# Kernel tuning notes

Hardware: AMD Instinct MI355X
Metric: run time of the kernel (lower is better)

Reference implementation:

```python
import jax, jax.numpy as jnp
import numpy as np
import math

DIM = 128
K = 64
OUT = 256
N, H, W = 32, 64, 64
EPS = 1e-12  # F.normalize clamp


def _l2norm(v, axis):
    n = jnp.sqrt(jnp.sum(v * v, axis=axis, keepdims=True))
    return v / jnp.maximum(n, EPS)


def setup_inputs() -> dict:
    key = jax.random.key(0)
    ks = jax.random.split(key, 6)
    s = 1.0 / math.sqrt(DIM)
    x = jax.random.normal(ks[0], (N, DIM, H, W), dtype=jnp.float32)
    cluster_centers = jax.random.uniform(ks[1], (K, DIM), dtype=jnp.float32) * s
    conv_w = jax.random.normal(ks[2], (K, DIM), dtype=jnp.float32) * s  # 1x1 conv kernel squeezed
    conv_b = jax.random.normal(ks[3], (K,), dtype=jnp.float32) * s
    mlp_w = jax.random.normal(ks[4], (OUT, K * DIM), dtype=jnp.float32) * s / math.sqrt(K * DIM)
    mlp_b = jax.random.normal(ks[5], (OUT,), dtype=jnp.float32) * s
    return {"x": x, "cluster_centers": cluster_centers, "conv_w": conv_w,
            "conv_b": conv_b, "mlp_w": mlp_w, "mlp_b": mlp_b}


def reference(x, cluster_centers, conv_w, conv_b, mlp_w, mlp_b):
    n, c, h, w = x.shape
    xf = x.reshape(n, c, h * w)                                   # [N,C,P]
    # 1x1 conv == per-pixel matmul
    logits = jnp.einsum('kc,ncp->nkp', conv_w, xf) + conv_b[None, :, None]
    a = jax.nn.softmax(logits, axis=1)                            # softmax over clusters, [N,K,P]
    # VLAD via algebraic identity (same math as broadcast-subtract-sum):
    # sum_p a[n,k,p]*(x[n,c,p] - centers[k,c])
    vlad = jnp.einsum('nkp,ncp->nkc', a, xf) \
           - a.sum(axis=-1)[..., None] * cluster_centers[None]    # [N,K,C]
    vlad = _l2norm(vlad, axis=2)            # intra-normalization over C
    vlad = vlad.reshape(n, -1)              # [N, K*C]
    vlad = _l2norm(vlad, axis=1)
    vlad = vlad @ mlp_w.T + mlp_b           # [N, OUT]
    vlad = _l2norm(vlad, axis=1)
    return vlad
```

## Files before the change

### kernel.cpp

```cpp
#include <hip/hip_runtime.h>
#include <math.h>


#define N_IMG 32
#define C_DIM 128
#define P_PIX 4096
#define K_CL  64
#define OUT_D 256

#define CHUNKS 8
#define NSUB 4
#define PART_ROW 132
#define PART_BLK (K_CL * PART_ROW)

typedef __attribute__((ext_vector_type(8))) short bf16x8;
typedef __attribute__((ext_vector_type(4))) short bf16x4;
typedef __attribute__((ext_vector_type(4))) float f32x4;
typedef __attribute__((ext_vector_type(2))) unsigned u32x2;
typedef __attribute__((ext_vector_type(4))) unsigned u32x4;

__device__ __forceinline__ unsigned cvtpk(float a, float b) {
    unsigned r;
    asm("v_cvt_pk_bf16_f32 %0, %1, %2" : "=v"(r) : "v"(a), "v"(b));
    return r;
}
__device__ __forceinline__ unsigned short bf1(float a) {
    union { float f; unsigned u; } x; x.f = a;
    return (unsigned short)((x.u + 0x7FFFu + ((x.u >> 16) & 1u)) >> 16);
}

__device__ __forceinline__ f32x4 mfma16(bf16x8 a, bf16x8 b, f32x4 c) {
    return __builtin_amdgcn_mfma_f32_16x16x32_bf16(a, b, c, 0, 0, 0);
}

__device__ __forceinline__ u32x2 tr16(unsigned addr) {
    u32x2 d;
    asm volatile("ds_read_b64_tr_b16 %0, %1" : "=v"(d) : "v"(addr));
    return d;
}
__device__ __forceinline__ u32x2 tr16_o1024(unsigned addr) {
    u32x2 d;
    asm volatile("ds_read_b64_tr_b16 %0, %1 offset:1024" : "=v"(d) : "v"(addr));
    return d;
}

__device__ __forceinline__ void bar_lgkm() {
    __builtin_amdgcn_sched_barrier(0);
    asm volatile("s_waitcnt lgkmcnt(0)" ::: "memory");
    __builtin_amdgcn_s_barrier();
    __builtin_amdgcn_sched_barrier(0);
}

template<int CTRL>
__device__ __forceinline__ float dppmv(float v) {
    union { float f; int i; } u; u.f = v;
    u.i = __builtin_amdgcn_update_dpp(u.i, u.i, CTRL, 0xF, 0xF, false);
    return u.f;
}
__device__ __forceinline__ float rowmax16(float v) {
    v = fmaxf(v, dppmv<0xB1>(v));
    v = fmaxf(v, dppmv<0x4E>(v));
    v = fmaxf(v, dppmv<0x141>(v));
    v = fmaxf(v, dppmv<0x140>(v));
    return v;
}
__device__ __forceinline__ float rowsum16(float v) {
    v += dppmv<0xB1>(v);
    v += dppmv<0x4E>(v);
    v += dppmv<0x141>(v);
    v += dppmv<0x140>(v);
    return v;
}

__global__ __launch_bounds__(512, 2)
void k_vlad_mfma(const float* __restrict__ x, const float* __restrict__ conv_w,
                 const float* __restrict__ conv_b, float* __restrict__ part)
{
    __shared__ short xc_s[16384];
    __shared__ short a_s[8192];
    __shared__ short w_s[8192];
    __shared__ float asred[512];

    const int t   = threadIdx.x;
    const int w   = t >> 6;
    const int l   = t & 63;
    const int l15 = l & 15;
    const int lg  = l >> 4;
    const int n   = blockIdx.x >> 3;
    const int ch  = blockIdx.x & 7;
    const int pb0 = ch * 512;

    const unsigned xc_base = (unsigned)(unsigned long long)(void*)xc_s;
    const float LOG2E = 1.44269504f;

    const float* xr0 = x + ((long)n * C_DIM + 16 * w + l15) * P_PIX;
    float4 raw[8];
#pragma unroll
    for (int ks = 0; ks < 4; ++ks) {
        const float* p = xr0 + pb0 + ks * 32 + lg * 8;
        raw[ks * 2 + 0] = *(const float4*)(p);
        raw[ks * 2 + 1] = *(const float4*)(p + 4);
    }

    {
        const int k = t >> 3, sub = t & 7;
        const float* wr = conv_w + k * C_DIM + sub * 16;
#pragma unroll
        for (int j = 0; j < 2; ++j) {
            float4 a = *(const float4*)(wr + j * 8);
            float4 b = *(const float4*)(wr + j * 8 + 4);
            union { u32x4 u; bf16x8 v; } cv;
            cv.u.x = cvtpk(a.x * LOG2E, a.y * LOG2E);
            cv.u.y = cvtpk(a.z * LOG2E, a.w * LOG2E);
            cv.u.z = cvtpk(b.x * LOG2E, b.y * LOG2E);
            cv.u.w = cvtpk(b.z * LOG2E, b.w * LOG2E);
            const int g = sub * 2 + j;
            const unsigned off = (unsigned)(k * 256 + ((g * 16) ^ ((k & 7) << 4)));
            *(bf16x8*)((char*)w_s + off) = cv.v;
        }
    }
    float bias[4];
#pragma unroll
    for (int nt = 0; nt < 4; ++nt) bias[nt] = conv_b[nt * 16 + l15] * LOG2E;

    bar_lgkm();

    bf16x8 wf[4][4];
#pragma unroll
    for (int nt = 0; nt < 4; ++nt)
#pragma unroll
        for (int ks = 0; ks < 4; ++ks) {
            const unsigned wb = (unsigned)((nt * 16 + l15) * 256
                + ((ks * 64 + lg * 16) ^ ((l15 & 7) << 4)));
            wf[nt][ks] = *(const bf16x8*)((char*)w_s + wb);
        }

    f32x4 acc2[4];
#pragma unroll
    for (int mt = 0; mt < 4; ++mt) acc2[mt] = (f32x4){0.f, 0.f, 0.f, 0.f};
    float asum[4] = {0.f, 0.f, 0.f, 0.f};
    bf16x8 oct[4];

#pragma unroll
    for (int s = 0; s < NSUB; ++s) {
#pragma unroll
        for (int ks = 0; ks < 4; ++ks) {
            const float4 A = raw[ks * 2];
            const float4 B = raw[ks * 2 + 1];
            union { u32x4 u; bf16x8 v; } cv;
            cv.u.x = cvtpk(A.x, A.y); cv.u.y = cvtpk(A.z, A.w);
            cv.u.z = cvtpk(B.x, B.y); cv.u.w = cvtpk(B.z, B.w);
            oct[ks] = cv.v;
        }
#pragma unroll
        for (int ks = 0; ks < 4; ++ks) {
            const int c  = 16 * w + l15;
            const int pl = ks * 32 + lg * 8;
            const unsigned off = (unsigned)((c >> 2) * 1024 + (pl >> 4) * 128
                                            + (c & 3) * 32 + (pl & 15) * 2);
            *(bf16x8*)((char*)xc_s + off) = oct[ks];
        }
        if (s + 1 < NSUB) {
#pragma unroll
            for (int ks = 0; ks < 4; ++ks) {
                const float* p = xr0 + pb0 + (s + 1) * 128 + ks * 32 + lg * 8;
                raw[ks * 2 + 0] = *(const float4*)(p);
                raw[ks * 2 + 1] = *(const float4*)(p + 4);
            }
        }
        bar_lgkm();

        u32x2 trr[4][2];
#pragma unroll
        for (int ks = 0; ks < 4; ++ks) {
            const unsigned ab = xc_base
                + (unsigned)((ks * 8 + lg * 2) * 1024 + l15 * 2 + w * 128);
            trr[ks][0] = tr16(ab);
            trr[ks][1] = tr16_o1024(ab);
        }
        asm volatile("s_waitcnt lgkmcnt(0)" ::: "memory");
        __builtin_amdgcn_sched_barrier(0);

        f32x4 acc1[4];
#pragma unroll
        for (int nt = 0; nt < 4; ++nt) acc1[nt] = (f32x4){0.f, 0.f, 0.f, 0.f};
#pragma unroll
        for (int ks = 0; ks < 4; ++ks) {
            union { u32x4 u; bf16x8 v; } a0;
            a0.u = (u32x4){trr[ks][0].x, trr[ks][0].y, trr[ks][1].x, trr[ks][1].y};
#pragma unroll
            for (int nt = 0; nt < 4; ++nt)
                acc1[nt] = mfma16(a0.v, wf[nt][ks], acc1[nt]);
        }

#pragma unroll
        for (int r = 0; r < 4; ++r) {
            float v0 = acc1[0][r] + bias[0];
            float v1 = acc1[1][r] + bias[1];
            float v2 = acc1[2][r] + bias[2];
            float v3 = acc1[3][r] + bias[3];
            float m = fmaxf(fmaxf(v0, v1), fmaxf(v2, v3));
            m = rowmax16(m);
            v0 = exp2f(v0 - m); v1 = exp2f(v1 - m);
            v2 = exp2f(v2 - m); v3 = exp2f(v3 - m);
            float sm = (v0 + v1) + (v2 + v3);
            sm = rowsum16(sm);
            const float inv = __builtin_amdgcn_rcpf(sm);
            v0 *= inv; v1 *= inv; v2 *= inv; v3 *= inv;
            asum[0] += v0; asum[1] += v1; asum[2] += v2; asum[3] += v3;
            acc1[0][r] = v0; acc1[1][r] = v1; acc1[2][r] = v2; acc1[3][r] = v3;
        }

        {
            const int pbyte = w * 32 + lg * 8;
#pragma unroll
            for (int nt = 0; nt < 4; ++nt) {
                const int k = nt * 16 + l15;
                union { u32x2 u; bf16x4 v; } pk4;
                pk4.u.x = cvtpk(acc1[nt][0], acc1[nt][1]);
                pk4.u.y = cvtpk(acc1[nt][2], acc1[nt][3]);
                const unsigned off =
                    (unsigned)(k * 256 + (pbyte ^ ((k & 7) << 4)));
                *(bf16x4*)((char*)a_s + off) = pk4.v;
            }
        }
        bar_lgkm();

#pragma unroll
        for (int ks = 0; ks < 4; ++ks) {
            bf16x8 af[4];
#pragma unroll
            for (int mt = 0; mt < 4; ++mt) {
                const int k = mt * 16 + l15;
                const unsigned off = (unsigned)(k * 256
                    + ((ks * 64 + lg * 16) ^ ((k & 7) << 4)));
                af[mt] = *(const bf16x8*)((char*)a_s + off);
            }
#pragma unroll
            for (int mt = 0; mt < 4; ++mt)
                acc2[mt] = mfma16(af[mt], oct[ks], acc2[mt]);
        }
    }

    const long pbase = (long)blockIdx.x * PART_BLK;
    {
        const int c = 16 * w + l15;
#pragma unroll
        for (int mt = 0; mt < 4; ++mt)
#pragma unroll
            for (int r = 0; r < 4; ++r) {
                const int k = mt * 16 + lg * 4 + r;
                part[pbase + (long)k * PART_ROW + c] = acc2[mt][r];
            }
    }
#pragma unroll
    for (int nt = 0; nt < 4; ++nt) {
        float a = asum[nt];
        a += __shfl_xor(a, 16);
        a += __shfl_xor(a, 32);
        if (lg == 0) asred[w * 64 + nt * 16 + l15] = a;
    }
    __syncthreads();
    if (t < 64) {
        float a = 0.f;
#pragma unroll
        for (int j = 0; j < 8; ++j) a += asred[j * 64 + t];
        part[pbase + (long)t * PART_ROW + 128] = a;
    }
}

__global__ __launch_bounds__(128)
void k_reduce_norm(const float* __restrict__ part, const float* __restrict__ centers,
                   unsigned short* __restrict__ vn16, float* __restrict__ rsq)
{
    const int b = blockIdx.x;
    const int n = b >> 6, k = b & 63;
    const int c = threadIdx.x;
    float acc = 0.f, as = 0.f;
#pragma unroll
    for (int ch = 0; ch < CHUNKS; ++ch) {
        const float* p = part + ((long)(n * CHUNKS + ch) * PART_BLK + k * PART_ROW);
        acc += p[c];
        as  += p[128];
    }
    const float v = fmaf(-as, centers[k * C_DIM + c], acc);
    float sq = v * v;
#pragma unroll
    for (int m = 1; m < 64; m <<= 1) sq += __shfl_xor(sq, m);
    __shared__ float red[2];
    if ((c & 63) == 0) red[c >> 6] = sq;
    __syncthreads();
    const float total = red[0] + red[1];
    const float s = 1.0f / fmaxf(sqrtf(total), 1e-12f);
    vn16[(long)n * 8192 + k * C_DIM + c] = bf1(v * s);
    if (c == 0) rsq[n * K_CL + k] = total * s * s;
}

__global__ __launch_bounds__(256)
void k_mlp_mfma(const unsigned short* __restrict__ vn16,
                const float* __restrict__ mlp_w, float* __restrict__ part2)
{
    __shared__ short wt[8192];
    __shared__ short vt[8192];

    const int t  = threadIdx.x;
    const int og = blockIdx.x & 7;
    const int jc = blockIdx.x >> 3;
    const int j0 = jc * 256;

    {
        const int r = t >> 3, sub = t & 7;
        const float* wp = mlp_w + (long)(og * 32 + r) * 8192 + j0;
#pragma unroll
        for (int i = 0; i < 8; ++i) {
            const int jl = i * 32 + sub * 4;
            float4 a = *(const float4*)(wp + jl);
            union { u32x2 u; bf16x4 v; } cv;
            cv.u.x = cvtpk(a.x, a.y);
            cv.u.y = cvtpk(a.z, a.w);
            const unsigned off = (unsigned)(r * 512 + ((jl * 2) ^ ((r & 7) << 4)));
            *(bf16x4*)((char*)wt + off) = cv.v;
        }
    }
    {
        const int r = t >> 3, sub = t & 7;
        const unsigned short* vp = vn16 + (long)r * 8192 + j0;
#pragma unroll
        for (int i = 0; i < 4; ++i) {
            const int jl = i * 64 + sub * 8;
            bf16x8 v = *(const bf16x8*)(vp + jl);
            const unsigned off = (unsigned)(r * 512 + ((jl * 2) ^ ((r & 7) << 4)));
            *(bf16x8*)((char*)vt + off) = v;
        }
    }
    __syncthreads();

    const int w = t >> 6, l = t & 63, l15 = l & 15, lg = l >> 4;
    const int mt = w >> 1, ot = w & 1;
    f32x4 acc = (f32x4){0.f, 0.f, 0.f, 0.f};
#pragma unroll
    for (int kk = 0; kk < 8; ++kk) {
        const int rowa = mt * 16 + l15;
        const int rowb = ot * 16 + l15;
        const int jb = (kk * 32 + lg * 8) * 2;
        bf16x8 af = *(const bf16x8*)((char*)vt
                        + (unsigned)(rowa * 512 + (jb ^ ((rowa & 7) << 4))));
        bf16x8 bf = *(const bf16x8*)((char*)wt
                        + (unsigned)(rowb * 512 + (jb ^ ((rowb & 7) << 4))));
        acc = mfma16(af, bf, acc);
    }
#pragma unroll
    for (int r = 0; r < 4; ++r) {
        const int nn = mt * 16 + lg * 4 + r;
        const int oo = og * 32 + ot * 16 + l15;
        part2[(long)nn * 8192 + jc * 256 + oo] = acc[r];
    }
}

__global__ __launch_bounds__(1024)
void k_finalize(const float* __restrict__ part2, const float* __restrict__ mlp_b,
                const float* __restrict__ rsq, float* __restrict__ out)
{
    __shared__ float psum[4][256];
    __shared__ float red[4];
    const int n = blockIdx.x;
    const int t = threadIdx.x;
    const int o = t & 255, q = t >> 8;

    float acc = 0.f;
#pragma unroll
    for (int j = 0; j < 8; ++j)
        acc += part2[(long)n * 8192 + (q * 8 + j) * 256 + o];
    psum[q][o] = acc;
    __syncthreads();

    float y = 0.f;
    if (q == 0) {
        float g = 0.f;
#pragma unroll
        for (int i = 0; i < 16; ++i) {
            const float4 r = *(const float4*)&rsq[n * K_CL + i * 4];
            g += r.x + r.y + r.z + r.w;
        }
        const float s = 1.0f / fmaxf(sqrtf(g), 1e-12f);
        const float tot = psum[0][o] + psum[1][o] + psum[2][o] + psum[3][o];
        y = fmaf(tot * s, 1.0f, mlp_b[o]);
        float sq = y * y;
#pragma unroll
        for (int m = 1; m < 64; m <<= 1) sq += __shfl_xor(sq, m);
        if ((o & 63) == 0) red[o >> 6] = sq;
    }
    __syncthreads();
    if (q == 0) {
        const float tot2 = red[0] + red[1] + red[2] + red[3];
        out[n * OUT_D + o] = y / fmaxf(sqrtf(tot2), 1e-12f);
    }
}

extern "C" void kernel_launch(void* const* d_in, const int* in_sizes, int n_in,
                              void* d_out, int out_size, void* d_ws, size_t ws_size,
                              hipStream_t stream)
{
    const float* x       = (const float*)d_in[0];
    const float* centers = (const float*)d_in[1];
    const float* conv_w  = (const float*)d_in[2];
    const float* conv_b  = (const float*)d_in[3];
    const float* mlp_w   = (const float*)d_in[4];
    const float* mlp_b   = (const float*)d_in[5];

    float* ws = (float*)d_ws;
    float* part = ws;
    unsigned short* vn16 = (unsigned short*)(part + 256 * PART_BLK);
    float* rsq   = (float*)(vn16 + 32 * 8192);
    float* part2 = rsq + 2048;

    k_vlad_mfma<<<dim3(256), dim3(512), 0, stream>>>(x, conv_w, conv_b, part);
    k_reduce_norm<<<dim3(2048), dim3(128), 0, stream>>>(part, centers, vn16, rsq);
    k_mlp_mfma<<<dim3(256), dim3(256), 0, stream>>>(vn16, mlp_w, part2);
    k_finalize<<<dim3(32), dim3(1024), 0, stream>>>(part2, mlp_b, rsq, (float*)d_out);
}
```

Baseline: 35.54 us.

## Software-pipeline x sub-chunk conversion and LDS staging across loop iterations

Peels the first sub-chunk's bf16 conversion, LDS store and next global prefetch out of the loop. Inside the loop, the next sub-chunk is converted before the second MFMA stage and written to LDS after it, and the prefetch two steps ahead is issued there. The goal is to overlap conversion, LDS writes and global loads with MFMA work instead of serialising them at the top of each iteration. The catch is more live registers (noct alongside oct and raw), and the xc_s write after the MFMAs relies on the barrier ordering being correct.

```diff
diff --git a/kernel.cpp b/kernel.cpp
--- a/kernel.cpp
+++ b/kernel.cpp
@@ -141,8 +141,7 @@
     float asum[4] = {0.f, 0.f, 0.f, 0.f};
     bf16x8 oct[4];
 
-#pragma unroll
-    for (int s = 0; s < NSUB; ++s) {
+    {
 #pragma unroll
         for (int ks = 0; ks < 4; ++ks) {
             const float4 A = raw[ks * 2];
@@ -152,22 +151,24 @@
             cv.u.z = cvtpk(B.x, B.y); cv.u.w = cvtpk(B.z, B.w);
             oct[ks] = cv.v;
         }
-#pragma unroll
-        for (int ks = 0; ks < 4; ++ks) {
-            const int c  = 16 * w + l15;
+        const int c = 16 * w + l15;
+#pragma unroll
+        for (int ks = 0; ks < 4; ++ks) {
             const int pl = ks * 32 + lg * 8;
             const unsigned off = (unsigned)((c >> 2) * 1024 + (pl >> 4) * 128
                                             + (c & 3) * 32 + (pl & 15) * 2);
             *(bf16x8*)((char*)xc_s + off) = oct[ks];
         }
-        if (s + 1 < NSUB) {
-#pragma unroll
-            for (int ks = 0; ks < 4; ++ks) {
-                const float* p = xr0 + pb0 + (s + 1) * 128 + ks * 32 + lg * 8;
-                raw[ks * 2 + 0] = *(const float4*)(p);
-                raw[ks * 2 + 1] = *(const float4*)(p + 4);
-            }
-        }
+#pragma unroll
+        for (int ks = 0; ks < 4; ++ks) {
+            const float* p = xr0 + pb0 + 128 + ks * 32 + lg * 8;
+            raw[ks * 2 + 0] = *(const float4*)(p);
+            raw[ks * 2 + 1] = *(const float4*)(p + 4);
+        }
+    }
+
+#pragma unroll
+    for (int s = 0; s < NSUB; ++s) {
         bar_lgkm();
 
         u32x2 trr[4][2];
@@ -226,6 +227,18 @@
         }
         bar_lgkm();
 
+        bf16x8 noct[4];
+        if (s + 1 < NSUB) {
+#pragma unroll
+            for (int ks = 0; ks < 4; ++ks) {
+                const float4 A = raw[ks * 2];
+                const float4 B = raw[ks * 2 + 1];
+                union { u32x4 u; bf16x8 v; } cv;
+                cv.u.x = cvtpk(A.x, A.y); cv.u.y = cvtpk(A.z, A.w);
+                cv.u.z = cvtpk(B.x, B.y); cv.u.w = cvtpk(B.z, B.w);
+                noct[ks] = cv.v;
+            }
+        }
 #pragma unroll
         for (int ks = 0; ks < 4; ++ks) {
             bf16x8 af[4];
@@ -239,6 +252,25 @@
 #pragma unroll
             for (int mt = 0; mt < 4; ++mt)
                 acc2[mt] = mfma16(af[mt], oct[ks], acc2[mt]);
+        }
+        if (s + 1 < NSUB) {
+            const int c = 16 * w + l15;
+#pragma unroll
+            for (int ks = 0; ks < 4; ++ks) {
+                const int pl = ks * 32 + lg * 8;
+                const unsigned off = (unsigned)((c >> 2) * 1024 + (pl >> 4) * 128
+                                                + (c & 3) * 32 + (pl & 15) * 2);
+                *(bf16x8*)((char*)xc_s + off) = noct[ks];
+                oct[ks] = noct[ks];
+            }
+            if (s + 2 < NSUB) {
+#pragma unroll
+                for (int ks = 0; ks < 4; ++ks) {
+                    const float* p = xr0 + pb0 + (s + 2) * 128 + ks * 32 + lg * 8;
+                    raw[ks * 2 + 0] = *(const float4*)(p);
+                    raw[ks * 2 + 1] = *(const float4*)(p + 4);
+                }
+            }
         }
     }
 
```

After: 35.47 us, median of 2. No clear change (-0.2%).

## Double pixel sub-tile size to halve sub-iterations and barriers

Applied to the files above, without the earlier changes.

Each block now processes 256 pixels per sub-iteration instead of 128, with two sub-iterations instead of four. This doubles the register prefetch buffer, the bf16 staging tiles in LDS and the per-wave MFMA work, so there are fewer barrier round trips and more independent MFMAs between barriers. In exchange it uses more registers and LDS, which may lower occupancy below the two blocks per CU set by the launch bounds, and it loses some of the overlap of global loads with compute.

```diff
diff --git a/kernel.cpp b/kernel.cpp
--- a/kernel.cpp
+++ b/kernel.cpp
@@ -9,7 +9,7 @@
 #define OUT_D 256
 
 #define CHUNKS 8
-#define NSUB 4
+#define NSUB 2
 #define PART_ROW 132
 #define PART_BLK (K_CL * PART_ROW)
 
@@ -38,9 +38,9 @@
     asm volatile("ds_read_b64_tr_b16 %0, %1" : "=v"(d) : "v"(addr));
     return d;
 }
-__device__ __forceinline__ u32x2 tr16_o1024(unsigned addr) {
+__device__ __forceinline__ u32x2 tr16_o2048(unsigned addr) {
     u32x2 d;
-    asm volatile("ds_read_b64_tr_b16 %0, %1 offset:1024" : "=v"(d) : "v"(addr));
+    asm volatile("ds_read_b64_tr_b16 %0, %1 offset:2048" : "=v"(d) : "v"(addr));
     return d;
 }
 
@@ -76,8 +76,8 @@
 void k_vlad_mfma(const float* __restrict__ x, const float* __restrict__ conv_w,
                  const float* __restrict__ conv_b, float* __restrict__ part)
 {
-    __shared__ short xc_s[16384];
-    __shared__ short a_s[8192];
+    __shared__ short xc_s[32768];
+    __shared__ short a_s[16384];
     __shared__ short w_s[8192];
     __shared__ float asred[512];
 
@@ -94,9 +94,9 @@
     const float LOG2E = 1.44269504f;
 
     const float* xr0 = x + ((long)n * C_DIM + 16 * w + l15) * P_PIX;
-    float4 raw[8];
-#pragma unroll
-    for (int ks = 0; ks < 4; ++ks) {
+    float4 raw[16];
+#pragma unroll
+    for (int ks = 0; ks < 8; ++ks) {
         const float* p = xr0 + pb0 + ks * 32 + lg * 8;
         raw[ks * 2 + 0] = *(const float4*)(p);
         raw[ks * 2 + 1] = *(const float4*)(p + 4);
@@ -139,12 +139,12 @@
 #pragma unroll
     for (int mt = 0; mt < 4; ++mt) acc2[mt] = (f32x4){0.f, 0.f, 0.f, 0.f};
     float asum[4] = {0.f, 0.f, 0.f, 0.f};
-    bf16x8 oct[4];
+    bf16x8 oct[8];
 
 #pragma unroll
     for (int s = 0; s < NSUB; ++s) {
 #pragma unroll
-        for (int ks = 0; ks < 4; ++ks) {
+        for (int ks = 0; ks < 8; ++ks) {
             const float4 A = raw[ks * 2];
             const float4 B = raw[ks * 2 + 1];
             union { u32x4 u; bf16x8 v; } cv;
@@ -152,87 +152,103 @@
             cv.u.z = cvtpk(B.x, B.y); cv.u.w = cvtpk(B.z, B.w);
             oct[ks] = cv.v;
         }
-#pragma unroll
-        for (int ks = 0; ks < 4; ++ks) {
-            const int c  = 16 * w + l15;
-            const int pl = ks * 32 + lg * 8;
-            const unsigned off = (unsigned)((c >> 2) * 1024 + (pl >> 4) * 128
-                                            + (c & 3) * 32 + (pl & 15) * 2);
-            *(bf16x8*)((char*)xc_s + off) = oct[ks];
+        {
+            const int c = 16 * w + l15;
+            const unsigned cb = (unsigned)((c >> 2) * 2048 + (c & 3) * 32);
+#pragma unroll
+            for (int ks = 0; ks < 8; ++ks) {
+                const int pl = ks * 32 + lg * 8;
+                const unsigned off = cb + (unsigned)((pl >> 4) * 128 + (pl & 15) * 2);
+                *(bf16x8*)((char*)xc_s + off) = oct[ks];
+            }
         }
         if (s + 1 < NSUB) {
 #pragma unroll
-            for (int ks = 0; ks < 4; ++ks) {
-                const float* p = xr0 + pb0 + (s + 1) * 128 + ks * 32 + lg * 8;
+            for (int ks = 0; ks < 8; ++ks) {
+                const float* p = xr0 + pb0 + 256 + ks * 32 + lg * 8;
                 raw[ks * 2 + 0] = *(const float4*)(p);
                 raw[ks * 2 + 1] = *(const float4*)(p + 4);
             }
         }
         bar_lgkm();
 
-        u32x2 trr[4][2];
-#pragma unroll
-        for (int ks = 0; ks < 4; ++ks) {
-            const unsigned ab = xc_base
-                + (unsigned)((ks * 8 + lg * 2) * 1024 + l15 * 2 + w * 128);
-            trr[ks][0] = tr16(ab);
-            trr[ks][1] = tr16_o1024(ab);
-        }
+        u32x2 trr[2][4][2];
+#pragma unroll
+        for (int pt2 = 0; pt2 < 2; ++pt2)
+#pragma unroll
+            for (int ks = 0; ks < 4; ++ks) {
+                const unsigned ab = xc_base
+                    + (unsigned)((ks * 8 + lg * 2) * 2048
+                                 + (2 * w + pt2) * 128 + l15 * 2);
+                trr[pt2][ks][0] = tr16(ab);
+                trr[pt2][ks][1] = tr16_o2048(ab);
+            }
         asm volatile("s_waitcnt lgkmcnt(0)" ::: "memory");
         __builtin_amdgcn_sched_barrier(0);
 
-        f32x4 acc1[4];
-#pragma unroll
-        for (int nt = 0; nt < 4; ++nt) acc1[nt] = (f32x4){0.f, 0.f, 0.f, 0.f};
-#pragma unroll
-        for (int ks = 0; ks < 4; ++ks) {
-            union { u32x4 u; bf16x8 v; } a0;
-            a0.u = (u32x4){trr[ks][0].x, trr[ks][0].y, trr[ks][1].x, trr[ks][1].y};
+        f32x4 acc1[2][4];
+#pragma unroll
+        for (int pt2 = 0; pt2 < 2; ++pt2)
 #pragma unroll
             for (int nt = 0; nt < 4; ++nt)
-                acc1[nt] = mfma16(a0.v, wf[nt][ks], acc1[nt]);
-        }
-
-#pragma unroll
-        for (int r = 0; r < 4; ++r) {
-            float v0 = acc1[0][r] + bias[0];
-            float v1 = acc1[1][r] + bias[1];
-            float v2 = acc1[2][r] + bias[2];
-            float v3 = acc1[3][r] + bias[3];
-            float m = fmaxf(fmaxf(v0, v1), fmaxf(v2, v3));
-            m = rowmax16(m);
-            v0 = exp2f(v0 - m); v1 = exp2f(v1 - m);
-            v2 = exp2f(v2 - m); v3 = exp2f(v3 - m);
-            float sm = (v0 + v1) + (v2 + v3);
-            sm = rowsum16(sm);
-            const float inv = __builtin_amdgcn_rcpf(sm);
-            v0 *= inv; v1 *= inv; v2 *= inv; v3 *= inv;
-            asum[0] += v0; asum[1] += v1; asum[2] += v2; asum[3] += v3;
-            acc1[0][r] = v0; acc1[1][r] = v1; acc1[2][r] = v2; acc1[3][r] = v3;
-        }
-
-        {
-            const int pbyte = w * 32 + lg * 8;
+                acc1[pt2][nt] = (f32x4){0.f, 0.f, 0.f, 0.f};
+#pragma unroll
+        for (int pt2 = 0; pt2 < 2; ++pt2)
+#pragma unroll
+            for (int ks = 0; ks < 4; ++ks) {
+                union { u32x4 u; bf16x8 v; } a0;
+                a0.u = (u32x4){trr[pt2][ks][0].x, trr[pt2][ks][0].y,
+                               trr[pt2][ks][1].x, trr[pt2][ks][1].y};
+#pragma unroll
+                for (int nt = 0; nt < 4; ++nt)
+                    acc1[pt2][nt] = mfma16(a0.v, wf[nt][ks], acc1[pt2][nt]);
+            }
+
+#pragma unroll
+        for (int pt2 = 0; pt2 < 2; ++pt2) {
+#pragma unroll
+            for (int r = 0; r < 4; ++r) {
+                float v0 = acc1[pt2][0][r] + bias[0];
+                float v1 = acc1[pt2][1][r] + bias[1];
+                float v2 = acc1[pt2][2][r] + bias[2];
+                float v3 = acc1[pt2][3][r] + bias[3];
+                float m = fmaxf(fmaxf(v0, v1), fmaxf(v2, v3));
+                m = rowmax16(m);
+                v0 = exp2f(v0 - m); v1 = exp2f(v1 - m);
+                v2 = exp2f(v2 - m); v3 = exp2f(v3 - m);
+                float sm = (v0 + v1) + (v2 + v3);
+                sm = rowsum16(sm);
+                const float inv = __builtin_amdgcn_rcpf(sm);
+                v0 *= inv; v1 *= inv; v2 *= inv; v3 *= inv;
+                asum[0] += v0; asum[1] += v1; asum[2] += v2; asum[3] += v3;
+                acc1[pt2][0][r] = v0; acc1[pt2][1][r] = v1;
+                acc1[pt2][2][r] = v2; acc1[pt2][3][r] = v3;
+            }
+        }
+
+#pragma unroll
+        for (int pt2 = 0; pt2 < 2; ++pt2) {
+            const int pbyte = (2 * w + pt2) * 32 + lg * 8;
 #pragma unroll
             for (int nt = 0; nt < 4; ++nt) {
                 const int k = nt * 16 + l15;
                 union { u32x2 u; bf16x4 v; } pk4;
-                pk4.u.x = cvtpk(acc1[nt][0], acc1[nt][1]);
-                pk4.u.y = cvtpk(acc1[nt][2], acc1[nt][3]);
+                pk4.u.x = cvtpk(acc1[pt2][nt][0], acc1[pt2][nt][1]);
+                pk4.u.y = cvtpk(acc1[pt2][nt][2], acc1[pt2][nt][3]);
                 const unsigned off =
-                    (unsigned)(k * 256 + (pbyte ^ ((k & 7) << 4)));
+                    (unsigned)(k * 512 + (pbyte ^ ((k & 7) << 4)));
                 *(bf16x4*)((char*)a_s + off) = pk4.v;
             }
         }
         bar_lgkm();
 
 #pragma unroll
-        for (int ks = 0; ks < 4; ++ks) {
+        for (int ks = 0; ks < 8; ++ks) {
             bf16x8 af[4];
 #pragma unroll
             for (int mt = 0; mt < 4; ++mt) {
                 const int k = mt * 16 + l15;
-                const unsigned off = (unsigned)(k * 256
+                const unsigned off = (unsigned)(k * 512
                     + ((ks * 64 + lg * 16) ^ ((k & 7) << 4)));
                 af[mt] = *(const bf16x8*)((char*)a_s + off);
             }
```

New measurement: 39.86 us. +12.2%, slower.
